# Performance work log

Measured on AMD Instinct MI355X. Metric: run time of the kernel, lower is better.

## Reference

```python
import jax, jax.numpy as jnp
import numpy as np

B, I, H, O = 16384, 512, 1024, 512

def setup_inputs() -> dict:
    key = jax.random.key(0)
    ks = jax.random.split(key, 8)
    s_x = 1.0 / np.sqrt(I)
    s_h = 1.0 / np.sqrt(H)
    inp = jax.random.normal(ks[0], (B, I), jnp.float32)
    h = jax.random.normal(ks[1], (B, H), jnp.float32)
    c = jax.random.normal(ks[2], (B, H), jnp.float32)
    # stacked gate weights, order [i, o, f, z]
    Wx = jax.random.uniform(ks[3], (4, H, I), jnp.float32, -s_x, s_x)
    Wh = jax.random.uniform(ks[4], (4, H, H), jnp.float32, -s_h, s_h)
    # z-gate h2z weight is re-initialized with standard normal in reset_parameters
    Wh = Wh.at[3].set(jax.random.normal(ks[5], (H, H), jnp.float32))
    # biases per module init: i=linspace(-1,-10), o=0, f=linspace(1,10), z=0
    bx = jnp.stack([
        jnp.linspace(-1.0, -10.0, H, dtype=jnp.float32),
        jnp.zeros((H,), jnp.float32),
        jnp.linspace(1.0, 10.0, H, dtype=jnp.float32),
        jnp.zeros((H,), jnp.float32),
    ])
    Wout = jax.random.uniform(ks[6], (O, H), jnp.float32, -s_h, s_h)
    bout = jax.random.uniform(ks[7], (O,), jnp.float32, -s_h, s_h)
    return {"inp": inp, "h": h, "c": c, "Wx": Wx, "bx": bx, "Wh": Wh,
            "Wout": Wout, "bout": bout}

def reference(inp, h, c, Wx, bx, Wh, Wout, bout):
    # fused gate pre-activations: two stacked GEMMs
    # gx: [4, B, H], gh: [4, B, H]
    gx = jnp.einsum('bi,ghi->gbh', inp, Wx) + bx[:, None, :]
    gh = jnp.einsum('bh,gkh->gbk', h, Wh)
    g = gx + gh
    i = jax.nn.sigmoid(g[0])
    o = jax.nn.sigmoid(g[1])
    f = jax.nn.sigmoid(g[2])
    z = jnp.tanh(g[3])
    c_new = i * z + f * c
    h_new = o * jnp.tanh(c_new)  # act_fn = tanh
    out = h_new @ Wout.T + bout
    return (out, h_new)
```

## Files before the change

kernel.cpp:

```cpp
#include <hip/hip_runtime.h>
#include <stdint.h>

#define BB 16384
#define II 512
#define HH 1024
#define OO 512

typedef short s16x8 __attribute__((ext_vector_type(8)));
typedef float f32x4 __attribute__((ext_vector_type(4)));

__device__ __forceinline__ unsigned short f2bf(float x) {
  union { float f; unsigned u; } v; v.f = x;
  return (unsigned short)((v.u + 0x7fffu + ((v.u >> 16) & 1u)) >> 16);
}
__device__ __forceinline__ float bf2f(unsigned short b) {
  union { unsigned u; float f; } v; v.u = ((unsigned)b) << 16;
  return v.f;
}
__device__ __forceinline__ float sigmoid_f(float x) {
  return 1.0f / (1.0f + __expf(-x));
}
__device__ __forceinline__ float tanh_f(float x) {
  float ax = fabsf(x);
  float e = __expf(-2.0f * ax);
  float t = (1.0f - e) / (1.0f + e);
  return x >= 0.0f ? t : -t;
}

__device__ __forceinline__ void stage16(const void* g, void* l) {
  __builtin_amdgcn_global_load_lds((const __attribute__((address_space(1))) void*)g,
                                   (__attribute__((address_space(3))) void*)l,
                                   16, 0, 0);
}

__device__ __forceinline__ void mma_step64(const unsigned short* As, const unsigned short* Bs,
                                           f32x4 acc[4][4], int lane, int wave) {
  const int wm = wave & 1, wn = wave >> 1;
  const int ln = lane & 15, q = lane >> 4;
#pragma unroll
  for (int s = 0; s < 2; ++s) {
    s16x8 af[4], bfr[4];
#pragma unroll
    for (int i = 0; i < 4; ++i) {
      const int r = wm * 64 + i * 16 + ln;
      af[i] = *(const s16x8*)(As + r * 64 + ((((s << 2) + q) + r) & 7) * 8);
    }
#pragma unroll
    for (int i = 0; i < 4; ++i) {
      const int r = wn * 64 + i * 16 + ln;
      bfr[i] = *(const s16x8*)(Bs + r * 64 + ((((s << 2) + q) + r) & 7) * 8);
    }
#pragma unroll
    for (int mi = 0; mi < 4; ++mi)
#pragma unroll
      for (int ni = 0; ni < 4; ++ni)
        acc[mi][ni] = __builtin_amdgcn_mfma_f32_16x16x32_bf16(af[mi], bfr[ni], acc[mi][ni], 0, 0, 0);
  }
}


__global__ __launch_bounds__(256) void prep_X(const float* __restrict__ inp,
                                              const float* __restrict__ h,
                                              unsigned short* __restrict__ Xb,
                                              unsigned short* __restrict__ Hlo) {
  int t = blockIdx.x * 256 + threadIdx.x;
  int base = t * 8;
  int b = base / 1536;
  int k = base - b * 1536;
  const float* src = (k < 512) ? (inp + b * 512 + k) : (h + b * 1024 + (k - 512));
  float4 v0 = *(const float4*)src;
  float4 v1 = *(const float4*)(src + 4);
  float f[8] = {v0.x, v0.y, v0.z, v0.w, v1.x, v1.y, v1.z, v1.w};
  unsigned short hi[8];
#pragma unroll
  for (int i = 0; i < 8; ++i) hi[i] = f2bf(f[i]);
  *(s16x8*)(Xb + base) = *(s16x8*)hi;
  if (k >= 512) {
    unsigned short lo[8];
#pragma unroll
    for (int i = 0; i < 8; ++i) lo[i] = f2bf(f[i] - bf2f(hi[i]));
    *(s16x8*)(Hlo + b * 1024 + (k - 512)) = *(s16x8*)lo;
  }
}

__global__ __launch_bounds__(256) void prep_Wg(const float* __restrict__ Wx,
                                               const float* __restrict__ Wh,
                                               unsigned short* __restrict__ Wg) {
  int t = blockIdx.x * 256 + threadIdx.x;
  int base = t * 8;
  int n = base / 1536;
  int k = base - n * 1536;
  int r = n & 255;
  int gate = (r >> 4) & 3;
  int unit = ((n >> 8) << 6) + (((r >> 6) & 3) << 4) + (r & 15);
  const float* src = (k < 512) ? (Wx + (gate * 1024 + unit) * 512 + k)
                               : (Wh + (gate * 1024 + unit) * 1024 + (k - 512));
  float4 v0 = *(const float4*)src;
  float4 v1 = *(const float4*)(src + 4);
  float f[8] = {v0.x, v0.y, v0.z, v0.w, v1.x, v1.y, v1.z, v1.w};
  unsigned short o[8];
#pragma unroll
  for (int i = 0; i < 8; ++i) o[i] = f2bf(f[i]);
  *(s16x8*)(Wg + base) = *(s16x8*)o;
}

__global__ __launch_bounds__(256) void prep_Wz2(const float* __restrict__ Whz,
                                                unsigned short* __restrict__ Wz2) {
  int t = blockIdx.x * 256 + threadIdx.x;
  int base = t * 8;
  int n = base >> 11;
  int k = base & 2047;
  int klo = (k < 1024) ? k : (k - 1024);
  const float* src = Whz + n * 1024 + klo;
  float4 v0 = *(const float4*)src;
  float4 v1 = *(const float4*)(src + 4);
  float f[8] = {v0.x, v0.y, v0.z, v0.w, v1.x, v1.y, v1.z, v1.w};
  unsigned short o[8];
  if (k < 1024) {
#pragma unroll
    for (int i = 0; i < 8; ++i) { unsigned short h_ = f2bf(f[i]); o[i] = f2bf(f[i] - bf2f(h_)); }
  } else {
#pragma unroll
    for (int i = 0; i < 8; ++i) o[i] = f2bf(f[i]);
  }
  *(s16x8*)(Wz2 + base) = *(s16x8*)o;
}

__global__ __launch_bounds__(256) void prep_Wout(const float* __restrict__ Wout,
                                                 unsigned short* __restrict__ Wo) {
  int t = blockIdx.x * 256 + threadIdx.x;
  int base = t * 8;
  float4 v0 = *(const float4*)(Wout + base);
  float4 v1 = *(const float4*)(Wout + base + 4);
  float f[8] = {v0.x, v0.y, v0.z, v0.w, v1.x, v1.y, v1.z, v1.w};
  unsigned short o[8];
#pragma unroll
  for (int i = 0; i < 8; ++i) o[i] = f2bf(f[i]);
  *(s16x8*)(Wo + base) = *(s16x8*)o;
}


#define RD_A(CA, MI, KS) (*(const s16x8*)((CA) + ((KS) ? aoff1 : aoff0) + (MI) * 1024))
#define RD_B(CB, NI, KS) (*(const s16x8*)((CB) + ((KS) ? boff1 : boff0) + (NI) * 1024))
#define VM8 asm volatile("s_waitcnt vmcnt(8)" ::: "memory")
#define VM0 asm volatile("s_waitcnt vmcnt(0)" ::: "memory")
#define LGKM0 asm volatile("s_waitcnt lgkmcnt(0)" ::: "memory")
#define VMNONE ((void)0)
#define NOST ((void)0)

#define ST_A2(TT, DB) do { \
  stage16(gA[0][0] + (size_t)(TT) * 64, (DB)); \
  stage16(gA[0][1] + (size_t)(TT) * 64, (DB) + 4096); \
  stage16(gA[1][0] + (size_t)(TT) * 64, (DB) + 8192); \
  stage16(gA[1][1] + (size_t)(TT) * 64, (DB) + 12288); } while (0)
#define ST_B2(TT, DB) do { \
  stage16(gB[0][0] + (size_t)(TT) * 64, (DB)); \
  stage16(gB[0][1] + (size_t)(TT) * 64, (DB) + 4096); \
  stage16(gB[1][0] + (size_t)(TT) * 64, (DB) + 8192); \
  stage16(gB[1][1] + (size_t)(TT) * 64, (DB) + 12288); } while (0)
#define ZST_A2(TT, DB) do { \
  const unsigned short *z0_, *z1_, *z2_, *z3_; \
  if ((TT) < 16) { \
    z0_ = gAX[0][0] + (size_t)(TT) * 64; z1_ = gAX[0][1] + (size_t)(TT) * 64; \
    z2_ = gAX[1][0] + (size_t)(TT) * 64; z3_ = gAX[1][1] + (size_t)(TT) * 64; \
  } else { \
    const int tz_ = (TT) - 16; \
    z0_ = gAH[0][0] + (size_t)tz_ * 64; z1_ = gAH[0][1] + (size_t)tz_ * 64; \
    z2_ = gAH[1][0] + (size_t)tz_ * 64; z3_ = gAH[1][1] + (size_t)tz_ * 64; \
  } \
  stage16(z0_, (DB)); stage16(z1_, (DB) + 4096); \
  stage16(z2_, (DB) + 8192); stage16(z3_, (DB) + 12288); } while (0)

#define PH(Q, WAIT, A00, A01, A10, A11) do { \
  __builtin_amdgcn_s_barrier(); \
  WAIT; \
  __builtin_amdgcn_sched_barrier(0); \
  __builtin_amdgcn_s_setprio(1); \
  _Pragma("unroll") \
  for (int ni = 0; ni < 4; ++ni) { \
    acc[2 * (Q)    ][ni] = __builtin_amdgcn_mfma_f32_16x16x32_bf16(A00, bq0[ni], acc[2 * (Q)    ][ni], 0, 0, 0); \
    acc[2 * (Q) + 1][ni] = __builtin_amdgcn_mfma_f32_16x16x32_bf16(A01, bq0[ni], acc[2 * (Q) + 1][ni], 0, 0, 0); \
  } \
  _Pragma("unroll") \
  for (int ni = 0; ni < 4; ++ni) { \
    acc[2 * (Q)    ][ni] = __builtin_amdgcn_mfma_f32_16x16x32_bf16(A10, bq1[ni], acc[2 * (Q)    ][ni], 0, 0, 0); \
    acc[2 * (Q) + 1][ni] = __builtin_amdgcn_mfma_f32_16x16x32_bf16(A11, bq1[ni], acc[2 * (Q) + 1][ni], 0, 0, 0); \
  } \
  __builtin_amdgcn_s_setprio(0); \
} while (0)

#define KTILE2(CA, CB, SB2, SA2, VMX) do { \
  s16x8 bq0[4], bq1[4], p0[4], p1[4]; \
  _Pragma("unroll") \
  for (int ni = 0; ni < 4; ++ni) { bq0[ni] = RD_B(CB, ni, 0); bq1[ni] = RD_B(CB, ni, 1); } \
  _Pragma("unroll") \
  for (int mi = 0; mi < 4; ++mi) { p0[mi] = RD_A(CA, mi, 0); p1[mi] = RD_A(CA, mi, 1); } \
  PH(0, LGKM0, p0[0], p0[1], p1[0], p1[1]); \
  __builtin_amdgcn_s_barrier(); \
  s16x8 r0[4], r1[4]; \
  _Pragma("unroll") \
  for (int mi = 0; mi < 4; ++mi) { r0[mi] = RD_A(CA, 4 + mi, 0); r1[mi] = RD_A(CA, 4 + mi, 1); } \
  SB2; \
  PH(1, VMNONE, p0[2], p0[3], p1[2], p1[3]); \
  __builtin_amdgcn_s_barrier(); \
  PH(2, LGKM0, r0[0], r0[1], r1[0], r1[1]); \
  __builtin_amdgcn_s_barrier(); \
  SA2; \
  PH(3, VMNONE, r0[2], r0[3], r1[2], r1[3]); \
  VMX; \
  __builtin_amdgcn_s_barrier(); \
} while (0)

__global__ __launch_bounds__(512, 2) void gemm_gates2(const unsigned short* __restrict__ Xb,
                                                      const unsigned short* __restrict__ Wg,
                                                      const float* __restrict__ bx,
                                                      const float* __restrict__ cold,
                                                      const unsigned short* __restrict__ Dgz,
                                                      float* __restrict__ hnew,
                                                      unsigned short* __restrict__ hnewb) {
  __shared__ unsigned short lds[2][2][16384];
  const int tid = threadIdx.x;
  const int lane = tid & 63, wave = tid >> 6;
  const int wm = wave & 1, wn = wave >> 1;
  const int ln = lane & 15, qlane = lane >> 4;
  const int fid = (int)(blockIdx.y * 16 + blockIdx.x);
  const int swz = ((fid & 7) << 7) + (fid >> 3);
  const int bxi = swz & 15, byi = swz >> 4;
  const int n0 = bxi << 8, m0 = byi << 8;
  const int sr = tid >> 3;
  const int j = ((tid & 7) - (sr & 7)) & 7;

  const unsigned short* gA[2][2];
  const unsigned short* gB[2][2];
#pragma unroll
  for (int hh = 0; hh < 2; ++hh)
#pragma unroll
    for (int u = 0; u < 2; ++u) {
      const int row = hh * 128 + u * 64 + sr;
      gA[hh][u] = Xb + (size_t)(m0 + row) * 1536 + j * 8;
      gB[hh][u] = Wg + (size_t)(n0 + row) * 1536 + j * 8;
    }
  unsigned short* const dA0 = &lds[0][0][0] + (tid & ~63) * 8;
  unsigned short* const dB0 = &lds[0][1][0] + (tid & ~63) * 8;
  unsigned short* const dA1 = &lds[1][0][0] + (tid & ~63) * 8;
  unsigned short* const dB1 = &lds[1][1][0] + (tid & ~63) * 8;
  const unsigned short* const lA0 = &lds[0][0][0];
  const unsigned short* const lB0 = &lds[0][1][0];
  const unsigned short* const lA1 = &lds[1][0][0];
  const unsigned short* const lB1 = &lds[1][1][0];
  const int sl0 = ((qlane + ln) & 7) * 8;
  const int sl1 = sl0 ^ 32;
  const int aoff0 = (wm * 128 + ln) * 64 + sl0;
  const int aoff1 = (wm * 128 + ln) * 64 + sl1;
  const int boff0 = (wn * 64 + ln) * 64 + sl0;
  const int boff1 = (wn * 64 + ln) * 64 + sl1;

  f32x4 acc[8][4] = {};

  ST_A2(0, dA0); ST_B2(0, dB0);
  ST_A2(1, dA1); ST_B2(1, dB1);
  VM8;
  __builtin_amdgcn_s_barrier();

#pragma unroll 1
  for (int t = 0; t < 22; t += 2) {
    KTILE2(lA0, lB0, ST_B2(t + 2, dB0), ST_A2(t + 2, dA0), VM8);
    KTILE2(lA1, lB1, ST_B2(t + 3, dB1), ST_A2(t + 3, dA1), VM8);
  }
  KTILE2(lA0, lB0, NOST, NOST, VM0);
  KTILE2(lA1, lB1, NOST, NOST, VMNONE);

  const int unit = (bxi << 6) + (wn << 4) + ln;
  const float bi = bx[unit];
  const float bo = bx[1024 + unit];
  const float bfg = bx[2048 + unit];
  const float bz = bx[3072 + unit];
#pragma unroll
  for (int mi = 0; mi < 8; ++mi) {
#pragma unroll
    for (int r = 0; r < 4; ++r) {
      const int b = m0 + wm * 128 + mi * 16 + qlane * 4 + r;
      const int idx = b * 1024 + unit;
      const float gi = acc[mi][0][r] + bi;
      const float go = acc[mi][1][r] + bo;
      const float gf = acc[mi][2][r] + bfg;
      const float gz = acc[mi][3][r] + bz + bf2f(Dgz[idx]);
      const float iv = sigmoid_f(gi);
      const float ov = sigmoid_f(go);
      const float fv = sigmoid_f(gf);
      const float zv = tanh_f(gz);
      const float cn = iv * zv + fv * cold[idx];
      const float hn = ov * tanh_f(cn);
      hnew[idx] = hn;
      hnewb[idx] = f2bf(hn);
    }
  }
}

__global__ __launch_bounds__(512, 2) void gemm_zcorr2(const unsigned short* __restrict__ Xb,
                                                      const unsigned short* __restrict__ Hlo,
                                                      const unsigned short* __restrict__ Wz2,
                                                      unsigned short* __restrict__ Dgz) {
  __shared__ unsigned short lds[2][2][16384];
  const int tid = threadIdx.x;
  const int lane = tid & 63, wave = tid >> 6;
  const int wm = wave & 1, wn = wave >> 1;
  const int ln = lane & 15, qlane = lane >> 4;
  const int fid = (int)(blockIdx.y * 4 + blockIdx.x);
  const int swz = ((fid & 7) << 5) + (fid >> 3);
  const int bxi = swz & 3, byi = swz >> 2;
  const int n0 = bxi << 8, m0 = byi << 8;
  const int sr = tid >> 3;
  const int j = ((tid & 7) - (sr & 7)) & 7;

  const unsigned short* gAX[2][2];
  const unsigned short* gAH[2][2];
  const unsigned short* gB[2][2];
#pragma unroll
  for (int hh = 0; hh < 2; ++hh)
#pragma unroll
    for (int u = 0; u < 2; ++u) {
      const int row = hh * 128 + u * 64 + sr;
      gAX[hh][u] = Xb  + (size_t)(m0 + row) * 1536 + 512 + j * 8;
      gAH[hh][u] = Hlo + (size_t)(m0 + row) * 1024 + j * 8;
      gB[hh][u]  = Wz2 + (size_t)(n0 + row) * 2048 + j * 8;
    }
  unsigned short* const dA0 = &lds[0][0][0] + (tid & ~63) * 8;
  unsigned short* const dB0 = &lds[0][1][0] + (tid & ~63) * 8;
  unsigned short* const dA1 = &lds[1][0][0] + (tid & ~63) * 8;
  unsigned short* const dB1 = &lds[1][1][0] + (tid & ~63) * 8;
  const unsigned short* const lA0 = &lds[0][0][0];
  const unsigned short* const lB0 = &lds[0][1][0];
  const unsigned short* const lA1 = &lds[1][0][0];
  const unsigned short* const lB1 = &lds[1][1][0];
  const int sl0 = ((qlane + ln) & 7) * 8;
  const int sl1 = sl0 ^ 32;
  const int aoff0 = (wm * 128 + ln) * 64 + sl0;
  const int aoff1 = (wm * 128 + ln) * 64 + sl1;
  const int boff0 = (wn * 64 + ln) * 64 + sl0;
  const int boff1 = (wn * 64 + ln) * 64 + sl1;

  f32x4 acc[8][4] = {};

  ZST_A2(0, dA0); ST_B2(0, dB0);
  ZST_A2(1, dA1); ST_B2(1, dB1);
  VM8;
  __builtin_amdgcn_s_barrier();

#pragma unroll 1
  for (int t = 0; t < 30; t += 2) {
    KTILE2(lA0, lB0, ST_B2(t + 2, dB0), ZST_A2(t + 2, dA0), VM8);
    KTILE2(lA1, lB1, ST_B2(t + 3, dB1), ZST_A2(t + 3, dA1), VM8);
  }
  KTILE2(lA0, lB0, NOST, NOST, VM0);
  KTILE2(lA1, lB1, NOST, NOST, VMNONE);

#pragma unroll
  for (int mi = 0; mi < 8; ++mi) {
#pragma unroll
    for (int r = 0; r < 4; ++r) {
      const int b = m0 + wm * 128 + mi * 16 + qlane * 4 + r;
#pragma unroll
      for (int ni = 0; ni < 4; ++ni) {
        const int n = n0 + wn * 64 + ni * 16 + ln;
        Dgz[b * 1024 + n] = f2bf(acc[mi][ni][r]);
      }
    }
  }
}

__global__ __launch_bounds__(256) void gemm_out(const unsigned short* __restrict__ Hb,
                                                const unsigned short* __restrict__ Wo,
                                                const float* __restrict__ bout,
                                                float* __restrict__ out) {
  __shared__ unsigned short As[8192];
  __shared__ unsigned short Bs[8192];
  const int fid = (int)(blockIdx.y * 4 + blockIdx.x);
  const int swz = ((fid & 7) << 6) + (fid >> 3);
  const int n0 = (swz & 3) * 128;
  const int m0 = (swz >> 2) * 128;
  const int tid = threadIdx.x, lane = tid & 63, wave = tid >> 6;
  const unsigned short *ga[4], *gb[4];
  unsigned short *la[4], *lb[4];
#pragma unroll
  for (int u = 0; u < 4; ++u) {
    int p = u * 256 + tid;
    int r = p >> 3;
    int jj = ((p & 7) - r) & 7;
    ga[u] = Hb + (size_t)(m0 + r) * 1024 + jj * 8;
    gb[u] = Wo + (size_t)(n0 + r) * 1024 + jj * 8;
    la[u] = As + (u * 256 + (tid & ~63)) * 8;
    lb[u] = Bs + (u * 256 + (tid & ~63)) * 8;
  }
  f32x4 acc[4][4] = {};
  for (int kk = 0; kk < 16; ++kk) {
#pragma unroll
    for (int u = 0; u < 4; ++u) { stage16(ga[u], la[u]); stage16(gb[u], lb[u]); }
#pragma unroll
    for (int u = 0; u < 4; ++u) { ga[u] += 64; gb[u] += 64; }
    __syncthreads();
    mma_step64(As, Bs, acc, lane, wave);
    __syncthreads();
  }
  const int wm = wave & 1, wn = wave >> 1;
  const int ln = lane & 15, q = lane >> 4;
  float bo_[4];
#pragma unroll
  for (int ni = 0; ni < 4; ++ni) bo_[ni] = bout[n0 + wn * 64 + ni * 16 + ln];
#pragma unroll
  for (int mi = 0; mi < 4; ++mi) {
#pragma unroll
    for (int r = 0; r < 4; ++r) {
      const int b = m0 + wm * 64 + mi * 16 + q * 4 + r;
#pragma unroll
      for (int ni = 0; ni < 4; ++ni) {
        const int n = n0 + wn * 64 + ni * 16 + ln;
        out[b * 512 + n] = acc[mi][ni][r] + bo_[ni];
      }
    }
  }
}

extern "C" void kernel_launch(void* const* d_in, const int* in_sizes, int n_in,
                              void* d_out, int out_size, void* d_ws, size_t ws_size,
                              hipStream_t stream) {
  const float* inp  = (const float*)d_in[0];
  const float* h    = (const float*)d_in[1];
  const float* c    = (const float*)d_in[2];
  const float* Wx   = (const float*)d_in[3];
  const float* bx   = (const float*)d_in[4];
  const float* Wh   = (const float*)d_in[5];
  const float* Wout = (const float*)d_in[6];
  const float* bout = (const float*)d_in[7];

  float* out  = (float*)d_out;
  float* hnew = out + (size_t)BB * OO;

  char* ws = (char*)d_ws;
  unsigned short* Xb  = (unsigned short*)(ws);
  unsigned short* Wg  = (unsigned short*)(ws + 50331648);
  unsigned short* Wo  = (unsigned short*)(ws + 62914560);
  unsigned short* Hb  = (unsigned short*)(ws + 63963136);
  unsigned short* Hlo = (unsigned short*)(ws + 97517568);
  unsigned short* Wz2 = (unsigned short*)(ws + 131072000);
  unsigned short* Dgz = (unsigned short*)(ws + 135266304);

  prep_X   <<<12288, 256, 0, stream>>>(inp, h, Xb, Hlo);
  prep_Wg  <<<3072,  256, 0, stream>>>(Wx, Wh, Wg);
  prep_Wz2 <<<1024,  256, 0, stream>>>(Wh + 3 * 1024 * 1024, Wz2);
  prep_Wout<<<256,   256, 0, stream>>>(Wout, Wo);
  gemm_zcorr2<<<dim3(4, 64),  512, 0, stream>>>(Xb, Hlo, Wz2, Dgz);
  gemm_gates2<<<dim3(16, 64), 512, 0, stream>>>(Xb, Wg, bx, c, Dgz, hnew, Hb);
  gemm_out  <<<dim3(4, 128),  256, 0, stream>>>(Hb, Wo, bout, out);
}
```

Measured before the change: 590.4 us.

## Software-pipeline LDS fragment reads across k-tiles and drop block swizzle

Restructures the GEMM main loop so A and B register fragments for the next quarter or next k-tile are read from LDS while the current MFMAs run. Waits become partial lgkmcnt/vmcnt counts instead of full drains, and the global-to-LDS staging is reshuffled across phases. It also removes the block-index swizzle in all three GEMM kernels and uses plain blockIdx mapping. This hides LDS latency behind MFMA work, but raises register pressure and may hurt L2 locality without the swizzle.

```diff
diff --git a/kernel.cpp b/kernel.cpp
--- a/kernel.cpp
+++ b/kernel.cpp
@@ -143,10 +143,21 @@
 #define RD_A(CA, MI, KS) (*(const s16x8*)((CA) + ((KS) ? aoff1 : aoff0) + (MI) * 1024))
 #define RD_B(CB, NI, KS) (*(const s16x8*)((CB) + ((KS) ? boff1 : boff0) + (NI) * 1024))
 #define VM8 asm volatile("s_waitcnt vmcnt(8)" ::: "memory")
+#define VM4 asm volatile("s_waitcnt vmcnt(4)" ::: "memory")
 #define VM0 asm volatile("s_waitcnt vmcnt(0)" ::: "memory")
+#define LGKM8 asm volatile("s_waitcnt lgkmcnt(8)" ::: "memory")
+#define LGKM4 asm volatile("s_waitcnt lgkmcnt(4)" ::: "memory")
 #define LGKM0 asm volatile("s_waitcnt lgkmcnt(0)" ::: "memory")
+#define BARR __builtin_amdgcn_s_barrier()
 #define VMNONE ((void)0)
 #define NOST ((void)0)
+
+#define AQ(S, CA, Q) do { \
+  S[0] = RD_A(CA, 2 * (Q), 0);  S[1] = RD_A(CA, 2 * (Q) + 1, 0); \
+  S[2] = RD_A(CA, 2 * (Q), 1);  S[3] = RD_A(CA, 2 * (Q) + 1, 1); } while (0)
+#define BH(BQ, CB, KS) do { \
+  BQ[4 * (KS) + 0] = RD_B(CB, 0, KS); BQ[4 * (KS) + 1] = RD_B(CB, 1, KS); \
+  BQ[4 * (KS) + 2] = RD_B(CB, 2, KS); BQ[4 * (KS) + 3] = RD_B(CB, 3, KS); } while (0)
 
 #define ST_A2(TT, DB) do { \
   stage16(gA[0][0] + (size_t)(TT) * 64, (DB)); \
@@ -171,44 +182,43 @@
   stage16(z0_, (DB)); stage16(z1_, (DB) + 4096); \
   stage16(z2_, (DB) + 8192); stage16(z3_, (DB) + 12288); } while (0)
 
-#define PH(Q, WAIT, A00, A01, A10, A11) do { \
+#define PH(Q, WAITM, S, BQ) do { \
   __builtin_amdgcn_s_barrier(); \
-  WAIT; \
+  WAITM; \
   __builtin_amdgcn_sched_barrier(0); \
   __builtin_amdgcn_s_setprio(1); \
   _Pragma("unroll") \
   for (int ni = 0; ni < 4; ++ni) { \
-    acc[2 * (Q)    ][ni] = __builtin_amdgcn_mfma_f32_16x16x32_bf16(A00, bq0[ni], acc[2 * (Q)    ][ni], 0, 0, 0); \
-    acc[2 * (Q) + 1][ni] = __builtin_amdgcn_mfma_f32_16x16x32_bf16(A01, bq0[ni], acc[2 * (Q) + 1][ni], 0, 0, 0); \
+    acc[2 * (Q)    ][ni] = __builtin_amdgcn_mfma_f32_16x16x32_bf16(S[0], BQ[ni], acc[2 * (Q)    ][ni], 0, 0, 0); \
+    acc[2 * (Q) + 1][ni] = __builtin_amdgcn_mfma_f32_16x16x32_bf16(S[1], BQ[ni], acc[2 * (Q) + 1][ni], 0, 0, 0); \
   } \
   _Pragma("unroll") \
   for (int ni = 0; ni < 4; ++ni) { \
-    acc[2 * (Q)    ][ni] = __builtin_amdgcn_mfma_f32_16x16x32_bf16(A10, bq1[ni], acc[2 * (Q)    ][ni], 0, 0, 0); \
-    acc[2 * (Q) + 1][ni] = __builtin_amdgcn_mfma_f32_16x16x32_bf16(A11, bq1[ni], acc[2 * (Q) + 1][ni], 0, 0, 0); \
+    acc[2 * (Q)    ][ni] = __builtin_amdgcn_mfma_f32_16x16x32_bf16(S[2], BQ[4 + ni], acc[2 * (Q)    ][ni], 0, 0, 0); \
+    acc[2 * (Q) + 1][ni] = __builtin_amdgcn_mfma_f32_16x16x32_bf16(S[3], BQ[4 + ni], acc[2 * (Q) + 1][ni], 0, 0, 0); \
   } \
   __builtin_amdgcn_s_setprio(0); \
 } while (0)
 
-#define KTILE2(CA, CB, SB2, SA2, VMX) do { \
-  s16x8 bq0[4], bq1[4], p0[4], p1[4]; \
-  _Pragma("unroll") \
-  for (int ni = 0; ni < 4; ++ni) { bq0[ni] = RD_B(CB, ni, 0); bq1[ni] = RD_B(CB, ni, 1); } \
-  _Pragma("unroll") \
-  for (int mi = 0; mi < 4; ++mi) { p0[mi] = RD_A(CA, mi, 0); p1[mi] = RD_A(CA, mi, 1); } \
-  PH(0, LGKM0, p0[0], p0[1], p1[0], p1[1]); \
-  __builtin_amdgcn_s_barrier(); \
-  s16x8 r0[4], r1[4]; \
-  _Pragma("unroll") \
-  for (int mi = 0; mi < 4; ++mi) { r0[mi] = RD_A(CA, 4 + mi, 0); r1[mi] = RD_A(CA, 4 + mi, 1); } \
-  SB2; \
-  PH(1, VMNONE, p0[2], p0[3], p1[2], p1[3]); \
-  __builtin_amdgcn_s_barrier(); \
-  PH(2, LGKM0, r0[0], r0[1], r1[0], r1[1]); \
-  __builtin_amdgcn_s_barrier(); \
-  SA2; \
-  PH(3, VMNONE, r0[2], r0[3], r1[2], r1[3]); \
-  VMX; \
-  __builtin_amdgcn_s_barrier(); \
+#define KT_STD(CA, CAn, CBn, BQC, BQN, AST, BST, VMQ1, VMQ2) do { \
+  AQ(aN, CA, 1); AST; \
+  PH(0, LGKM4, aC, BQC); BARR; \
+  AQ(aC, CA, 2); BST; \
+  PH(1, LGKM4, aN, BQC); VMQ1; BARR; \
+  AQ(aN, CA, 3); BH(BQN, CBn, 0); \
+  PH(2, LGKM8, aC, BQC); VMQ2; BARR; \
+  BH(BQN, CBn, 1); AQ(aC, CAn, 0); \
+  PH(3, LGKM8, aN, BQC); BARR; \
+} while (0)
+
+#define KT_LAST(CA, BQC) do { \
+  AQ(aN, CA, 1); \
+  PH(0, LGKM4, aC, BQC); BARR; \
+  AQ(aC, CA, 2); \
+  PH(1, LGKM4, aN, BQC); BARR; \
+  AQ(aN, CA, 3); \
+  PH(2, LGKM4, aC, BQC); BARR; \
+  PH(3, LGKM0, aN, BQC); \
 } while (0)
 
 __global__ __launch_bounds__(512, 2) void gemm_gates2(const unsigned short* __restrict__ Xb,
@@ -223,10 +233,7 @@
   const int lane = tid & 63, wave = tid >> 6;
   const int wm = wave & 1, wn = wave >> 1;
   const int ln = lane & 15, qlane = lane >> 4;
-  const int fid = (int)(blockIdx.y * 16 + blockIdx.x);
-  const int swz = ((fid & 7) << 7) + (fid >> 3);
-  const int bxi = swz & 15, byi = swz >> 4;
-  const int n0 = bxi << 8, m0 = byi << 8;
+  const int n0 = blockIdx.x << 8, m0 = blockIdx.y << 8;
   const int sr = tid >> 3;
   const int j = ((tid & 7) - (sr & 7)) & 7;
 
@@ -256,21 +263,26 @@
   const int boff1 = (wn * 64 + ln) * 64 + sl1;
 
   f32x4 acc[8][4] = {};
+  s16x8 aC[4], aN[4], bqA[8], bqB[8];
 
   ST_A2(0, dA0); ST_B2(0, dB0);
   ST_A2(1, dA1); ST_B2(1, dB1);
   VM8;
-  __builtin_amdgcn_s_barrier();
-
+  BARR;
+  BH(bqA, lB0, 0); BH(bqA, lB0, 1);
+  AQ(aC, lA0, 0);
+
+  KT_STD(lA0, lA1, lB1, bqA, bqB, NOST, ST_B2(2, dB0), VM4, VM4);
 #pragma unroll 1
-  for (int t = 0; t < 22; t += 2) {
-    KTILE2(lA0, lB0, ST_B2(t + 2, dB0), ST_A2(t + 2, dA0), VM8);
-    KTILE2(lA1, lB1, ST_B2(t + 3, dB1), ST_A2(t + 3, dA1), VM8);
-  }
-  KTILE2(lA0, lB0, NOST, NOST, VM0);
-  KTILE2(lA1, lB1, NOST, NOST, VMNONE);
-
-  const int unit = (bxi << 6) + (wn << 4) + ln;
+  for (int t = 1; t < 21; t += 2) {
+    KT_STD(lA1, lA0, lB0, bqB, bqA, ST_A2(t + 1, dA0), ST_B2(t + 2, dB1), VM8, VM4);
+    KT_STD(lA0, lA1, lB1, bqA, bqB, ST_A2(t + 2, dA1), ST_B2(t + 3, dB0), VM8, VM4);
+  }
+  KT_STD(lA1, lA0, lB0, bqB, bqA, ST_A2(22, dA0), ST_B2(23, dB1), VM8, VM4);
+  KT_STD(lA0, lA1, lB1, bqA, bqB, ST_A2(23, dA1), NOST, VM4, VM0);
+  KT_LAST(lA1, bqB);
+
+  const int unit = ((int)blockIdx.x << 6) + (wn << 4) + ln;
   const float bi = bx[unit];
   const float bo = bx[1024 + unit];
   const float bfg = bx[2048 + unit];
@@ -306,10 +318,7 @@
   const int lane = tid & 63, wave = tid >> 6;
   const int wm = wave & 1, wn = wave >> 1;
   const int ln = lane & 15, qlane = lane >> 4;
-  const int fid = (int)(blockIdx.y * 4 + blockIdx.x);
-  const int swz = ((fid & 7) << 5) + (fid >> 3);
-  const int bxi = swz & 3, byi = swz >> 2;
-  const int n0 = bxi << 8, m0 = byi << 8;
+  const int n0 = blockIdx.x << 8, m0 = blockIdx.y << 8;
   const int sr = tid >> 3;
   const int j = ((tid & 7) - (sr & 7)) & 7;
 
@@ -341,19 +350,24 @@
   const int boff1 = (wn * 64 + ln) * 64 + sl1;
 
   f32x4 acc[8][4] = {};
+  s16x8 aC[4], aN[4], bqA[8], bqB[8];
 
   ZST_A2(0, dA0); ST_B2(0, dB0);
   ZST_A2(1, dA1); ST_B2(1, dB1);
   VM8;
-  __builtin_amdgcn_s_barrier();
-
+  BARR;
+  BH(bqA, lB0, 0); BH(bqA, lB0, 1);
+  AQ(aC, lA0, 0);
+
+  KT_STD(lA0, lA1, lB1, bqA, bqB, NOST, ST_B2(2, dB0), VM4, VM4);
 #pragma unroll 1
-  for (int t = 0; t < 30; t += 2) {
-    KTILE2(lA0, lB0, ST_B2(t + 2, dB0), ZST_A2(t + 2, dA0), VM8);
-    KTILE2(lA1, lB1, ST_B2(t + 3, dB1), ZST_A2(t + 3, dA1), VM8);
-  }
-  KTILE2(lA0, lB0, NOST, NOST, VM0);
-  KTILE2(lA1, lB1, NOST, NOST, VMNONE);
+  for (int t = 1; t < 29; t += 2) {
+    KT_STD(lA1, lA0, lB0, bqB, bqA, ZST_A2(t + 1, dA0), ST_B2(t + 2, dB1), VM8, VM4);
+    KT_STD(lA0, lA1, lB1, bqA, bqB, ZST_A2(t + 2, dA1), ST_B2(t + 3, dB0), VM8, VM4);
+  }
+  KT_STD(lA1, lA0, lB0, bqB, bqA, ZST_A2(30, dA0), ST_B2(31, dB1), VM8, VM4);
+  KT_STD(lA0, lA1, lB1, bqA, bqB, ZST_A2(31, dA1), NOST, VM4, VM0);
+  KT_LAST(lA1, bqB);
 
 #pragma unroll
   for (int mi = 0; mi < 8; ++mi) {
@@ -375,10 +389,8 @@
                                                 float* __restrict__ out) {
   __shared__ unsigned short As[8192];
   __shared__ unsigned short Bs[8192];
-  const int fid = (int)(blockIdx.y * 4 + blockIdx.x);
-  const int swz = ((fid & 7) << 6) + (fid >> 3);
-  const int n0 = (swz & 3) * 128;
-  const int m0 = (swz >> 2) * 128;
+  const int n0 = blockIdx.x * 128;
+  const int m0 = blockIdx.y * 128;
   const int tid = threadIdx.x, lane = tid & 63, wave = tid >> 6;
   const unsigned short *ga[4], *gb[4];
   unsigned short *la[4], *lb[4];
```

Measured after the change: 717.2 us. 1.21x slower.
